# Kernel optimization log

Hardware: AMD Instinct MI355X
Metric: run time of the kernel (lower is better)

The kernel has to match this reference:

```python
import jax, jax.numpy as jnp
import numpy as np
from jax import lax
from jax.scipy.special import ndtri
from jax.scipy.stats import norm

# Hyperparameters from __init__ defaults (num_inputs=8)
MU_A = 0.99          # sigmoid(logit_mu_a)
SIGMA_A = 0.1
A_MAX = 1.0          # truncation upper bound (module-level constant in repo)
SIGMASQ0 = 1.0       # initial-state variance (module-level constant in repo)
SIGMA_MU_X = 1.0
MU_W = 0.0
SIGMA_W = 1.0

S, T, D = 512, 8192, 8


def setup_inputs() -> dict:
    key = jax.random.key(0)
    ks = jax.random.split(key, 8)
    return dict(
        inputs=jax.random.normal(ks[0], (S, T, D), jnp.float32),
        eps_w=jax.random.normal(ks[1], (S, D), jnp.float32),
        u_a=jax.random.uniform(ks[2], (S,), jnp.float32, 1e-4, 1.0 - 1e-4),
        sigmasq=jax.random.uniform(ks[3], (S,), jnp.float32, 0.01, 0.3),
        eps_mu=jax.random.normal(ks[4], (S,), jnp.float32),
        eps_x0=jax.random.normal(ks[5], (S,), jnp.float32),
        eps_x=jax.random.normal(ks[6], (S, T), jnp.float32),
        u_bern=jax.random.uniform(ks[7], (S, T), jnp.float32),
    )


def reference(inputs, eps_w, u_a, sigmasq, eps_mu, eps_x0, eps_x, u_bern):
    # Per-subject parameter draws (reparameterized)
    w = MU_W + SIGMA_W * eps_w                              # [S, D]  Normal(mu_w, sigma_w)
    # TruncatedNormal(MU_A, SIGMA_A, 0, A_MAX) via inverse CDF
    alpha = (0.0 - MU_A) / SIGMA_A
    beta = (A_MAX - MU_A) / SIGMA_A
    Fa, Fb = norm.cdf(alpha), norm.cdf(beta)
    a = MU_A + SIGMA_A * ndtri(Fa + u_a * (Fb - Fa))        # [S]
    mu_x = SIGMA_MU_X * eps_mu                              # [S]  Normal(0, sigma_mu_x)
    b = mu_x * (1.0 - a)                                    # [S]
    x0 = mu_x + jnp.sqrt(SIGMASQ0) * eps_x0                 # [S]
    sd = jnp.sqrt(sigmasq)                                  # [S]

    # AR(1) latent scan over trials, vectorized over subjects.
    # Matches original: outputs collect x_t BEFORE the update, i.e. x_0..x_{T-1}.
    def step(x, eps_t):
        x_next = a * x + b + sd * eps_t
        return x_next, x

    _, xs = lax.scan(step, x0, eps_x.T)                     # xs: [T, S]
    x = xs.T                                                # [S, T]

    logits = x + jnp.einsum('std,sd->st', inputs, w)        # [S, T]
    y = (u_bern < jax.nn.sigmoid(logits)).astype(jnp.int32) # Bernoulli(logits) sample
    return x, y
```

## Files before the change

### kernel.cpp

```cpp
#include <hip/hip_runtime.h>
#include <cmath>

#define S_SUB 512
#define T_TR  8192
#define D_IN  8
#define BLK   1024
#define CH    (T_TR/BLK)
#define NW    (BLK/64)

typedef float f4 __attribute__((ext_vector_type(4)));

__global__ void setup_kernel(const float* __restrict__ u_a,
                             const float* __restrict__ sigmasq,
                             const float* __restrict__ eps_mu,
                             const float* __restrict__ eps_x0,
                             double Fa, double dF,
                             double* __restrict__ params) {
    int s = blockIdx.x * blockDim.x + threadIdx.x;
    if (s >= S_SUB) return;
    const double RS2 = 0.7071067811865476;
    const double S2  = 1.4142135623730951;
    const double ISQ = 0.3989422804014327;
    double p = fma((double)u_a[s], dF, Fa);
    double z = -S2 * erfcinv(2.0 * p);
    #pragma unroll
    for (int it = 0; it < 2; ++it) {
        double F   = 0.5 * erfc(-z * RS2);
        double pdf = exp(-0.5 * z * z) * ISQ;
        z -= (F - p) / pdf;
    }
    double a  = 0.99 + 0.1 * z;
    double mu = (double)eps_mu[s];
    double b  = mu * (1.0 - a);
    double x0 = mu + (double)eps_x0[s];
    double sd = sqrt((double)sigmasq[s]);
    params[4*s+0] = a;
    params[4*s+1] = b;
    params[4*s+2] = sd;
    params[4*s+3] = x0;
}

__global__ __launch_bounds__(BLK, 8) void mono_kernel(
    const float* __restrict__ inputs,
    const float* __restrict__ eps_w,
    const float* __restrict__ eps_x,
    const float* __restrict__ u_bern,
    const double* __restrict__ params,
    float* __restrict__ out_x,
    float* __restrict__ out_y)
{
    const int s    = blockIdx.x;
    const int tid  = threadIdx.x;
    const int lane = tid & 63;
    const int wid  = tid >> 6;

    __shared__ double2 wtot[NW];
    __shared__ double  xs[BLK * (CH + 1)];

    const size_t subjbase = (size_t)s * T_TR;
    const size_t base     = subjbase + (size_t)tid * CH;

    const f4* e4 = (const f4*)(eps_x + base);
    f4 o0 = e4[0];
    f4 o1 = e4[1];

    const double a  = params[4*s+0];
    const double b  = params[4*s+1];
    const double sd = params[4*s+2];
    const double x0 = params[4*s+3];

    float ev[CH];
    ev[0]=o0.x; ev[1]=o0.y; ev[2]=o0.z; ev[3]=o0.w;
    ev[4]=o1.x; ev[5]=o1.y; ev[6]=o1.z; ev[7]=o1.w;

    double A = 1.0, Bv = 0.0;
    #pragma unroll
    for (int j = 0; j < CH; ++j) {
        double c = fma(sd, (double)ev[j], b);
        Bv = fma(a, Bv, c);
        A *= a;
    }

    #pragma unroll
    for (int off = 1; off < 64; off <<= 1) {
        double pA = __shfl_up(A, off);
        double pB = __shfl_up(Bv, off);
        if (lane >= off) {
            Bv = fma(A, pB, Bv);
            A  = A * pA;
        }
    }
    if (lane == 63) wtot[wid] = make_double2(A, Bv);
    __syncthreads();

    double PA = 1.0, PB = 0.0;
    for (int w = 0; w < wid; ++w) {
        double2 t = wtot[w];
        PB = fma(t.x, PB, t.y);
        PA = t.x * PA;
    }
    double eA = __shfl_up(A, 1);
    double eB = __shfl_up(Bv, 1);
    if (lane == 0) { eA = 1.0; eB = 0.0; }
    double EB = fma(eA, PB, eB);
    double EA = eA * PA;
    double x  = fma(EA, x0, EB);

    #pragma unroll
    for (int j = 0; j < CH; ++j) {
        xs[tid * (CH + 1) + j] = x;
        double c = fma(sd, (double)ev[j], b);
        x = fma(a, x, c);
    }
    __syncthreads();

    const float* wp = eps_w + s * D_IN;
    const double w0 = (double)wp[0], w1 = (double)wp[1];
    const double w2 = (double)wp[2], w3 = (double)wp[3];
    const double w4 = (double)wp[4], w5 = (double)wp[5];
    const double w6 = (double)wp[6], w7 = (double)wp[7];

    float uv[CH];
    #pragma unroll
    for (int j = 0; j < CH; ++j)
        uv[j] = u_bern[subjbase + j * BLK + tid];

    const f4* in4 = (const f4*)(inputs + subjbase * D_IN);
    #pragma unroll
    for (int j = 0; j < CH; ++j) {
        const int t = j * BLK + tid;
        f4 i0 = in4[2*t];
        f4 i1 = in4[2*t + 1];
        double xv = xs[(t >> 3) * (CH + 1) + (t & 7)];
        double dot = fma((double)i0.x, w0,
                     fma((double)i0.y, w1,
                     fma((double)i0.z, w2,
                     fma((double)i0.w, w3,
                     fma((double)i1.x, w4,
                     fma((double)i1.y, w5,
                     fma((double)i1.z, w6, (double)i1.w * w7)))))));
        double L = xv + dot;
        double E = exp(-L);
        out_y[subjbase + t] = ((double)uv[j] * (1.0 + E) < 1.0) ? 1.0f : 0.0f;
        out_x[subjbase + t] = (float)xv;
    }
}

extern "C" void kernel_launch(void* const* d_in, const int* in_sizes, int n_in,
                              void* d_out, int out_size, void* d_ws, size_t ws_size,
                              hipStream_t stream) {
    const float* inputs  = (const float*)d_in[0];
    const float* eps_w   = (const float*)d_in[1];
    const float* u_a     = (const float*)d_in[2];
    const float* sigmasq = (const float*)d_in[3];
    const float* eps_mu  = (const float*)d_in[4];
    const float* eps_x0  = (const float*)d_in[5];
    const float* eps_x   = (const float*)d_in[6];
    const float* u_bern  = (const float*)d_in[7];

    float*  out    = (float*)d_out;
    double* params = (double*)d_ws;

    const double RS2 = 0.7071067811865476;
    const double Fa  = 0.5 * erfc(9.9 * RS2);
    const double Fb  = 0.5 * erfc(-0.1 * RS2);
    const double dF  = Fb - Fa;

    setup_kernel<<<2, 256, 0, stream>>>(u_a, sigmasq, eps_mu, eps_x0, Fa, dF, params);
    mono_kernel<<<S_SUB, BLK, 0, stream>>>(inputs, eps_w, eps_x, u_bern, params,
                                           out, out + (size_t)S_SUB * T_TR);
}
```

Before: 39.29 us.

## Fuse parameter setup into main kernel and vectorize epilogue loads and stores

Removes the separate setup kernel: thread 0 of each block computes the truncated-normal draw and per-subject parameters into shared memory, followed by a barrier. This drops one launch and the global round trip for params. The epilogue also changes so each thread handles 4 consecutive timesteps, loading u_bern and storing out_x/out_y as float4 vectors. The cost is a serial erfcinv/erfc computation on one thread at the start of every block, and the inputs reads per thread become strided by 4 timesteps.

```diff
diff --git a/kernel.cpp b/kernel.cpp
--- a/kernel.cpp
+++ b/kernel.cpp
@@ -10,42 +10,16 @@
 
 typedef float f4 __attribute__((ext_vector_type(4)));
 
-__global__ void setup_kernel(const float* __restrict__ u_a,
-                             const float* __restrict__ sigmasq,
-                             const float* __restrict__ eps_mu,
-                             const float* __restrict__ eps_x0,
-                             double Fa, double dF,
-                             double* __restrict__ params) {
-    int s = blockIdx.x * blockDim.x + threadIdx.x;
-    if (s >= S_SUB) return;
-    const double RS2 = 0.7071067811865476;
-    const double S2  = 1.4142135623730951;
-    const double ISQ = 0.3989422804014327;
-    double p = fma((double)u_a[s], dF, Fa);
-    double z = -S2 * erfcinv(2.0 * p);
-    #pragma unroll
-    for (int it = 0; it < 2; ++it) {
-        double F   = 0.5 * erfc(-z * RS2);
-        double pdf = exp(-0.5 * z * z) * ISQ;
-        z -= (F - p) / pdf;
-    }
-    double a  = 0.99 + 0.1 * z;
-    double mu = (double)eps_mu[s];
-    double b  = mu * (1.0 - a);
-    double x0 = mu + (double)eps_x0[s];
-    double sd = sqrt((double)sigmasq[s]);
-    params[4*s+0] = a;
-    params[4*s+1] = b;
-    params[4*s+2] = sd;
-    params[4*s+3] = x0;
-}
-
 __global__ __launch_bounds__(BLK, 8) void mono_kernel(
     const float* __restrict__ inputs,
     const float* __restrict__ eps_w,
+    const float* __restrict__ u_a,
+    const float* __restrict__ sigmasq,
+    const float* __restrict__ eps_mu,
+    const float* __restrict__ eps_x0,
     const float* __restrict__ eps_x,
     const float* __restrict__ u_bern,
-    const double* __restrict__ params,
+    double Fa, double dF,
     float* __restrict__ out_x,
     float* __restrict__ out_y)
 {
@@ -55,6 +29,7 @@
     const int wid  = tid >> 6;
 
     __shared__ double2 wtot[NW];
+    __shared__ double  pl[4];
     __shared__ double  xs[BLK * (CH + 1)];
 
     const size_t subjbase = (size_t)s * T_TR;
@@ -64,10 +39,30 @@
     f4 o0 = e4[0];
     f4 o1 = e4[1];
 
-    const double a  = params[4*s+0];
-    const double b  = params[4*s+1];
-    const double sd = params[4*s+2];
-    const double x0 = params[4*s+3];
+    if (tid == 0) {
+        const double RS2 = 0.7071067811865476;
+        const double S2  = 1.4142135623730951;
+        const double ISQ = 0.3989422804014327;
+        double p = fma((double)u_a[s], dF, Fa);
+        double z = -S2 * erfcinv(2.0 * p);
+        #pragma unroll
+        for (int it = 0; it < 2; ++it) {
+            double F   = 0.5 * erfc(-z * RS2);
+            double pdf = exp(-0.5 * z * z) * ISQ;
+            z -= (F - p) / pdf;
+        }
+        double a  = 0.99 + 0.1 * z;
+        double mu = (double)eps_mu[s];
+        pl[0] = a;
+        pl[1] = mu * (1.0 - a);
+        pl[2] = sqrt((double)sigmasq[s]);
+        pl[3] = mu + (double)eps_x0[s];
+    }
+    __syncthreads();
+    const double a  = pl[0];
+    const double b  = pl[1];
+    const double sd = pl[2];
+    const double x0 = pl[3];
 
     float ev[CH];
     ev[0]=o0.x; ev[1]=o0.y; ev[2]=o0.z; ev[3]=o0.w;
@@ -120,29 +115,35 @@
     const double w4 = (double)wp[4], w5 = (double)wp[5];
     const double w6 = (double)wp[6], w7 = (double)wp[7];
 
-    float uv[CH];
-    #pragma unroll
-    for (int j = 0; j < CH; ++j)
-        uv[j] = u_bern[subjbase + j * BLK + tid];
-
     const f4* in4 = (const f4*)(inputs + subjbase * D_IN);
     #pragma unroll
-    for (int j = 0; j < CH; ++j) {
-        const int t = j * BLK + tid;
-        f4 i0 = in4[2*t];
-        f4 i1 = in4[2*t + 1];
-        double xv = xs[(t >> 3) * (CH + 1) + (t & 7)];
-        double dot = fma((double)i0.x, w0,
-                     fma((double)i0.y, w1,
-                     fma((double)i0.z, w2,
-                     fma((double)i0.w, w3,
-                     fma((double)i1.x, w4,
-                     fma((double)i1.y, w5,
-                     fma((double)i1.z, w6, (double)i1.w * w7)))))));
-        double L = xv + dot;
-        double E = exp(-L);
-        out_y[subjbase + t] = ((double)uv[j] * (1.0 + E) < 1.0) ? 1.0f : 0.0f;
-        out_x[subjbase + t] = (float)xv;
+    for (int g = 0; g < CH/4; ++g) {
+        const int t0 = g * (BLK * 4) + tid * 4;
+        f4 ub = *(const f4*)(u_bern + subjbase + t0);
+        float ubk[4]; ubk[0]=ub.x; ubk[1]=ub.y; ubk[2]=ub.z; ubk[3]=ub.w;
+        float xk[4], yk[4];
+        #pragma unroll
+        for (int k = 0; k < 4; ++k) {
+            const int t = t0 + k;
+            f4 i0 = in4[2*t];
+            f4 i1 = in4[2*t+1];
+            double xv = xs[(t >> 3) * (CH + 1) + (t & 7)];
+            double dot = fma((double)i0.x, w0,
+                         fma((double)i0.y, w1,
+                         fma((double)i0.z, w2,
+                         fma((double)i0.w, w3,
+                         fma((double)i1.x, w4,
+                         fma((double)i1.y, w5,
+                         fma((double)i1.z, w6, (double)i1.w * w7)))))));
+            double L = xv + dot;
+            double E = exp(-L);
+            yk[k] = ((double)ubk[k] * (1.0 + E) < 1.0) ? 1.0f : 0.0f;
+            xk[k] = (float)xv;
+        }
+        f4 vx; vx.x=xk[0]; vx.y=xk[1]; vx.z=xk[2]; vx.w=xk[3];
+        f4 vy; vy.x=yk[0]; vy.y=yk[1]; vy.z=yk[2]; vy.w=yk[3];
+        *(f4*)(out_x + subjbase + t0) = vx;
+        *(f4*)(out_y + subjbase + t0) = vy;
     }
 }
 
@@ -158,15 +159,14 @@
     const float* eps_x   = (const float*)d_in[6];
     const float* u_bern  = (const float*)d_in[7];
 
-    float*  out    = (float*)d_out;
-    double* params = (double*)d_ws;
+    float* out = (float*)d_out;
 
     const double RS2 = 0.7071067811865476;
     const double Fa  = 0.5 * erfc(9.9 * RS2);
     const double Fb  = 0.5 * erfc(-0.1 * RS2);
     const double dF  = Fb - Fa;
 
-    setup_kernel<<<2, 256, 0, stream>>>(u_a, sigmasq, eps_mu, eps_x0, Fa, dF, params);
-    mono_kernel<<<S_SUB, BLK, 0, stream>>>(inputs, eps_w, eps_x, u_bern, params,
+    mono_kernel<<<S_SUB, BLK, 0, stream>>>(inputs, eps_w, u_a, sigmasq, eps_mu,
+                                           eps_x0, eps_x, u_bern, Fa, dF,
                                            out, out + (size_t)S_SUB * T_TR);
 }
```

Result: slower. 47.33 us (+20.5%).
